# Kernel optimization log

Hardware: AMD Instinct MI355X
Metric: run time of the kernel (lower is better)

## Reference

```python
import jax, jax.numpy as jnp
import numpy as np

R = 16  # hypernetwork low rank


def _gru(x, W_ih, W_hh, b_ih, b_hh):
    # torch-style GRU (gate order: reset, update, new), batch_first. x: (B,N,D) -> (B,N,H)
    H = W_hh.shape[1]
    xp = jnp.einsum('bnd,gd->bng', x, W_ih) + b_ih            # (B,N,3H), hoisted out of scan
    xp = jnp.moveaxis(xp, 1, 0)                               # (N,B,3H)

    def step(h, xpt):
        gh = h @ W_hh.T + b_hh
        ir, iz, inn = jnp.split(xpt, 3, axis=-1)
        hr, hz, hn = jnp.split(gh, 3, axis=-1)
        r = jax.nn.sigmoid(ir + hr)
        z = jax.nn.sigmoid(iz + hz)
        n = jnp.tanh(inn + r * hn)
        h = (1.0 - z) * n + z * h
        return h, h

    h0 = jnp.zeros((x.shape[0], H), x.dtype)
    _, hs = jax.lax.scan(step, h0, xp)
    return jnp.moveaxis(hs, 0, 1)


def _assoc_scan(inputs, gates):
    # h_t = gates_t * h_{t-1} + inputs_t along the last axis (parallel associative scan)
    def combine(left, right):
        a1, b1 = left
        a2, b2 = right
        return a1 * a2, b1 * a2 + b2
    _, h = jax.lax.associative_scan(combine, (gates, inputs), axis=-1)
    return h


def setup_inputs() -> dict:
    key = jax.random.key(0)
    ks = jax.random.split(key, 18)
    B, N, D = 4, 2048, 512
    H3, Dh, Do = 3 * D, 1024, 2 * R * D
    s = 0.05
    inp = {
        'residual_stream': jax.random.normal(ks[0], (B, N, D), jnp.float32),
        'eps': jax.random.normal(ks[1], (B, N, D), jnp.float32),
        'ap_W_ih': jax.random.normal(ks[2], (H3, D)) * s,
        'ap_W_hh': jax.random.normal(ks[3], (H3, D)) * s,
        'ap_b_ih': jax.random.normal(ks[4], (H3,)) * s,
        'ap_b_hh': jax.random.normal(ks[5], (H3,)) * s,
        'su_W_ih': jax.random.normal(ks[6], (H3, D)) * s,
        'su_W_hh': jax.random.normal(ks[7], (H3, D)) * s,
        'su_b_ih': jax.random.normal(ks[8], (H3,)) * s,
        'su_b_hh': jax.random.normal(ks[9], (H3,)) * s,
        'readout_W': jax.random.normal(ks[10], (2 * D, D)) * s,
        'readout_b': jax.random.normal(ks[11], (2 * D,)) * s,
        'beta_W': jax.random.normal(ks[12], (D, D)) * s,
        'dec_W1': jax.random.normal(ks[13], (Dh, D)) * s,
        'dec_b1': jax.random.normal(ks[14], (Dh,)) * s,
        'dec_W2': jax.random.normal(ks[15], (Do, Dh)) * s,
        'dec_b2': jax.random.normal(ks[16], (Do,)) * s,
    }
    return inp


def reference(residual_stream, eps, ap_W_ih, ap_W_hh, ap_b_ih, ap_b_hh,
              su_W_ih, su_W_hh, su_b_ih, su_b_hh, readout_W, readout_b,
              beta_W, dec_W1, dec_b1, dec_W2, dec_b2):
    # non-discovery path: discovery_phase=False, hard_switch=False
    B, N, D = residual_stream.shape

    # action proposer GRU + Readout (mean / log_var, reparameterized sample)
    h = _gru(residual_stream, ap_W_ih, ap_W_hh, ap_b_ih, ap_b_hh)
    action_dist = (h @ readout_W.T + readout_b).reshape(B, N, D, 2)
    mean, log_var = action_dist[..., 0], action_dist[..., 1]
    sampled_action = mean + jnp.exp(0.5 * log_var) * eps      # (B,N,D)

    # switching unit -> per-latent-dim switch gate beta in (0,1)
    su = _gru(residual_stream, su_W_ih, su_W_hh, su_b_ih, su_b_hh)
    switch_beta = jax.nn.sigmoid(su @ beta_W.T)               # (B,N,D)

    # rearrange 'b n d -> (b d) n'
    intent = jnp.moveaxis(sampled_action, 1, 2).reshape(B * D, N)
    beta = jnp.moveaxis(switch_beta, 1, 2).reshape(B * D, N)
    forget = 1.0 - beta
    gated = _assoc_scan(intent * forget, beta)                # h_t = beta_t*h_{t-1} + (intent*forget)_t
    gated = jnp.moveaxis(gated.reshape(B, D, N), 1, 2)        # (B,N,D)

    # decoder MLP (depth=1): Linear -> SiLU -> Linear
    hdec = jax.nn.silu(gated @ dec_W1.T + dec_b1)             # (B,N,1024)
    dout = hdec @ dec_W2.T + dec_b2                           # (B,N,2*R*D)

    # '... (two d r) -> two ... d r'
    w = dout.reshape(B, N, 2, D, R)
    w1, w2 = w[..., 0, :, :], w[..., 1, :, :]                 # (B,N,D,R) each

    # control_i = g_i * sum_j sum_r w1_{i r} w2_{j r}  (fused; avoids (B,N,D,D) materialization)
    s = w2.sum(axis=-2)                                       # (B,N,R)
    t = jnp.einsum('bndr,bnr->bnd', w1, s)                    # (B,N,D)
    control_signal = gated * t

    modified = residual_stream + control_signal
    vae_kl_loss = jnp.zeros((), residual_stream.dtype)
    return modified, action_dist, sampled_action, vae_kl_loss
```

## Files before the change

### kernel.cpp

```cpp
#include <hip/hip_runtime.h>
#include <hip/hip_bf16.h>

typedef unsigned short ushort_t;
typedef unsigned long long u64_t;
typedef __attribute__((ext_vector_type(4))) float f32x4;
typedef __attribute__((ext_vector_type(8))) short short8;
typedef __attribute__((ext_vector_type(4))) unsigned int u32x4;
typedef __attribute__((ext_vector_type(4))) ushort_t u16x4;

#define BB 4
#define NN 2048
#define DD 512
#define H3 1536
#define SENT 0x7FC0ull

__device__ __forceinline__ ushort_t f2bf(float f) {
    union { float f; unsigned u; } v; v.f = f;
    unsigned r = v.u + 0x7FFFu + ((v.u >> 16) & 1u);
    return (ushort_t)(r >> 16);
}
__device__ __forceinline__ float sigm(float x) { return 1.f / (1.f + __expf(-x)); }
__device__ __forceinline__ float tanhx(float x) { return 1.f - 2.f / (__expf(2.f * x) + 1.f); }
__device__ __forceinline__ f32x4 bf4_to_f32(u64_t v) {
    f32x4 r;
#pragma unroll
    for (int i = 0; i < 4; ++i) {
        union { unsigned u; float f; } c;
        c.u = (unsigned)((v >> (16 * i)) & 0xFFFFull) << 16;
        r[i] = c.f;
    }
    return r;
}

__global__ __launch_bounds__(256) void k_cvt(const float* __restrict__ src, ushort_t* __restrict__ dst, int n4) {
    int i = blockIdx.x * 256 + threadIdx.x;
    if (i < n4) {
        f32x4 f = *(const f32x4*)(src + 4 * (size_t)i);
        u16x4 u;
#pragma unroll
        for (int r = 0; r < 4; ++r) u[r] = f2bf(f[r]);
        *(u16x4*)(dst + 4 * (size_t)i) = u;
    }
}

__global__ __launch_bounds__(256) void k_fill(u32x4* __restrict__ dst, int n16) {
    int i = blockIdx.x * 256 + threadIdx.x;
    if (i < n16) dst[i] = (u32x4){0x7FC07FC0u, 0x7FC07FC0u, 0x7FC07FC0u, 0x7FC07FC0u};
}

__global__ __launch_bounds__(256) void k_w2s(const float* __restrict__ W2, const float* __restrict__ b2,
                                             ushort_t* __restrict__ W2s, float* __restrict__ b2s) {
    int gid = blockIdx.x * 256 + threadIdx.x;
    int r = gid >> 10, k = gid & 1023;
    float s = 0.f;
    for (int d = 0; d < 512; ++d) s += W2[(size_t)(8192 + d * 16 + r) * 1024 + k];
    W2s[r * 1024 + k] = f2bf(s);
    if (gid < 16) {
        float sb = 0.f;
        for (int d = 0; d < 512; ++d) sb += b2[8192 + d * 16 + gid];
        b2s[gid] = sb;
    }
}

template <int BIAS, int ACT, int OUTBF, int REMAP>
__global__ __launch_bounds__(256) void k_gemm(const ushort_t* __restrict__ A, const ushort_t* __restrict__ W,
                                              const float* __restrict__ bias, float* __restrict__ Cf,
                                              ushort_t* __restrict__ Cbf, int M, int N, int K) {
    __shared__ __align__(16) ushort_t As[128 * 72];
    __shared__ __align__(16) ushort_t Bs[128 * 72];
    const int tid = threadIdx.x;
    const int lane = tid & 63, wave = tid >> 6;
    const int col = lane & 15, g4 = lane >> 4;
    const int wm = wave >> 1, wn = wave & 1;
    const int m0 = blockIdx.y * 128, n0 = blockIdx.x * 128;

    f32x4 acc[4][4];
#pragma unroll
    for (int i = 0; i < 4; ++i)
#pragma unroll
        for (int j = 0; j < 4; ++j) acc[i][j] = (f32x4){0.f, 0.f, 0.f, 0.f};

    for (int k0 = 0; k0 < K; k0 += 64) {
#pragma unroll
        for (int c = 0; c < 4; ++c) {
            int cid = tid + 256 * c;
            int row = cid >> 3, c8 = cid & 7;
            u32x4 va = *(const u32x4*)(A + (size_t)(m0 + row) * K + k0 + c8 * 8);
            *(u32x4*)(&As[row * 72 + c8 * 8]) = va;
            u32x4 vb = (u32x4){0u, 0u, 0u, 0u};
            if (n0 + row < N) vb = *(const u32x4*)(W + (size_t)(n0 + row) * K + k0 + c8 * 8);
            *(u32x4*)(&Bs[row * 72 + c8 * 8]) = vb;
        }
        __syncthreads();
#pragma unroll
        for (int ks = 0; ks < 2; ++ks) {
            short8 af[4], bf_[4];
#pragma unroll
            for (int i = 0; i < 4; ++i)
                af[i] = *(const short8*)(&As[(wm * 64 + i * 16 + col) * 72 + ks * 32 + g4 * 8]);
#pragma unroll
            for (int j = 0; j < 4; ++j)
                bf_[j] = *(const short8*)(&Bs[(wn * 64 + j * 16 + col) * 72 + ks * 32 + g4 * 8]);
#pragma unroll
            for (int i = 0; i < 4; ++i)
#pragma unroll
                for (int j = 0; j < 4; ++j)
                    acc[i][j] = __builtin_amdgcn_mfma_f32_16x16x32_bf16(af[i], bf_[j], acc[i][j], 0, 0, 0);
        }
        __syncthreads();
    }
#pragma unroll
    for (int j = 0; j < 4; ++j) {
        int n = n0 + wn * 64 + j * 16 + col;
        if (n >= N) continue;
        float bv = 0.f;
        if (BIAS) bv = bias[n];
#pragma unroll
        for (int i = 0; i < 4; ++i) {
#pragma unroll
            for (int r = 0; r < 4; ++r) {
                int m = m0 + wm * 64 + i * 16 + g4 * 4 + r;
                size_t mr = REMAP ? ((size_t)(m & 3) * 2048 + (m >> 2)) : (size_t)m;
                float v = acc[i][j][r] + bv;
                if (ACT == 1) v = sigm(v);
                else if (ACT == 2) v = v * sigm(v);
                if (OUTBF) Cbf[mr * N + n] = f2bf(v);
                else Cf[mr * N + n] = v;
            }
        }
    }
}

__global__ __launch_bounds__(512, 1) void k_gru(const float* __restrict__ Whh0, const float* __restrict__ Whh1,
                                                const float* __restrict__ bhh0, const float* __restrict__ bhh1,
                                                const ushort_t* __restrict__ xpb0, const ushort_t* __restrict__ xpb1,
                                                ushort_t* __restrict__ hseq0, ushort_t* __restrict__ hseq1) {
    __shared__ __align__(16) ushort_t HB[2][4 * 520];
    const int gru = blockIdx.x >> 2;
    const int wg = blockIdx.x & 3;
    const float* Whh = gru ? Whh1 : Whh0;
    const float* bhh = gru ? bhh1 : bhh0;
    const ushort_t* xpb = gru ? xpb1 : xpb0;
    ushort_t* hseq = gru ? hseq1 : hseq0;

    const int tid = threadIdx.x;
    const int wave = tid >> 6, lane = tid & 63;
    const int col = lane & 15, g4 = lane >> 4;
    const int u = wg * 8 + wave;
    const int c0 = u * 16;

    const bool gvalid = (tid < 384);
    const int uo = tid >> 4;
    const int gu = (uo < wg * 8) ? uo : uo + 8;
    const int gb = (tid >> 2) & 3, gq = tid & 3;
    const int g_u64 = gu * 4 + gq;
    const int g_lds = gb * 520 + gu * 16 + gq * 4;

    short8 af[3][16];
#pragma unroll
    for (int m = 0; m < 3; ++m) {
        int grow = m * 512 + c0 + col;
        const float* wr = Whh + (size_t)grow * 512;
#pragma unroll
        for (int q = 0; q < 16; ++q) {
            int k = q * 32 + g4 * 8;
            f32x4 f0 = *(const f32x4*)(wr + k);
            f32x4 f1 = *(const f32x4*)(wr + k + 4);
            short8 v;
#pragma unroll
            for (int i = 0; i < 4; ++i) v[i] = (short)f2bf(f0[i]);
#pragma unroll
            for (int i = 0; i < 4; ++i) v[4 + i] = (short)f2bf(f1[i]);
            af[m][q] = v;
        }
    }

    const bool active = (col < 4);
    const int b = active ? col : 0;
    const int j0 = c0 + g4 * 4;
    f32x4 bhr = {0.f, 0.f, 0.f, 0.f}, bhz = bhr, bhn = bhr;
    if (active) {
        bhr = *(const f32x4*)(bhh + j0);
        bhz = *(const f32x4*)(bhh + 512 + j0);
        bhn = *(const f32x4*)(bhh + 1024 + j0);
    }
    float hold[4] = {0.f, 0.f, 0.f, 0.f};
    long long budget = 1LL << 21;

    u64_t xr8 = 0, xz8 = 0, xn8 = 0;
    if (active) {
        const ushort_t* xpt = xpb + ((size_t)b * NN) * 1536;
        xr8 = *(const u64_t*)(xpt + j0);
        xz8 = *(const u64_t*)(xpt + 512 + j0);
        xn8 = *(const u64_t*)(xpt + 1024 + j0);
    }

    for (int t = 0; t < NN; ++t) {
        u64_t xrn = 0, xzn = 0, xnn = 0;
        if (active && t + 1 < NN) {
            const ushort_t* xpt = xpb + ((size_t)b * NN + t + 1) * 1536;
            xrn = *(const u64_t*)(xpt + j0);
            xzn = *(const u64_t*)(xpt + 512 + j0);
            xnn = *(const u64_t*)(xpt + 1024 + j0);
        }
        if (t > 0) {
            if (gvalid) {
                const u64_t* gp = (const u64_t*)hseq + ((size_t)(t - 1) * 4 + gb) * 128 + g_u64;
                u64_t v = __hip_atomic_load(gp, __ATOMIC_RELAXED, __HIP_MEMORY_SCOPE_AGENT);
                while ((v & 0xFFFFull) == SENT && --budget >= 0)
                    v = __hip_atomic_load(gp, __ATOMIC_RELAXED, __HIP_MEMORY_SCOPE_AGENT);
                *(u64_t*)(&HB[(t - 1) & 1][g_lds]) = v;
            }
        }
        __syncthreads();
        f32x4 a0 = {0.f, 0.f, 0.f, 0.f}, a1 = a0, a2 = a0;
        if (t > 0) {
            const ushort_t* hb = &HB[(t - 1) & 1][(col & 3) * 520];
            short8 bf_[16];
#pragma unroll
            for (int q = 0; q < 16; ++q) bf_[q] = *(const short8*)(hb + q * 32 + g4 * 8);
#pragma unroll
            for (int q = 0; q < 16; ++q) {
                a0 = __builtin_amdgcn_mfma_f32_16x16x32_bf16(af[0][q], bf_[q], a0, 0, 0, 0);
                a1 = __builtin_amdgcn_mfma_f32_16x16x32_bf16(af[1][q], bf_[q], a1, 0, 0, 0);
                a2 = __builtin_amdgcn_mfma_f32_16x16x32_bf16(af[2][q], bf_[q], a2, 0, 0, 0);
            }
        }
        if (active) {
            f32x4 xr = bf4_to_f32(xr8), xz = bf4_to_f32(xz8), xn = bf4_to_f32(xn8);
            u16x4 pk;
#pragma unroll
            for (int r = 0; r < 4; ++r) {
                float rr = sigm(xr[r] + bhr[r] + a0[r]);
                float zz = sigm(xz[r] + bhz[r] + a1[r]);
                float nnv = tanhx(xn[r] + rr * (a2[r] + bhn[r]));
                float hv = (1.f - zz) * nnv + zz * hold[r];
                hold[r] = hv;
                pk[r] = f2bf(hv);
            }
            union { u16x4 p; u64_t u; } pc;
            pc.p = pk;
            __hip_atomic_store((u64_t*)(hseq + ((size_t)t * 4 + b) * 512 + j0), pc.u, __ATOMIC_RELAXED,
                               __HIP_MEMORY_SCOPE_AGENT);
            *(u64_t*)(&HB[t & 1][b * 520 + j0]) = pc.u;
        }
        xr8 = xrn; xz8 = xzn; xn8 = xnn;
    }
}

__global__ __launch_bounds__(256) void k_sample(const float* __restrict__ ad, const float* __restrict__ eps,
                                                float* __restrict__ out2, int n) {
    int i = blockIdx.x * 256 + threadIdx.x;
    if (i < n) {
        float mean = ad[2 * (size_t)i];
        float lv = ad[2 * (size_t)i + 1];
        out2[i] = mean + __expf(0.5f * lv) * eps[i];
    }
}

#define NC 32
#define LCH 64
__global__ __launch_bounds__(512) void k_scan1(const float* __restrict__ beta_tm, const float* __restrict__ intent,
                                               float* __restrict__ Asum, float* __restrict__ Bsum) {
    int d = threadIdx.x;
    int b = blockIdx.x / NC, c = blockIdx.x % NC;
    float A = 1.f, Bc = 0.f;
    for (int i = 0; i < LCH; ++i) {
        size_t t = (size_t)c * LCH + i;
        float a = beta_tm[(t * 4 + b) * 512 + d];
        float x = intent[((size_t)b * NN + t) * 512 + d] * (1.f - a);
        A *= a;
        Bc = a * Bc + x;
    }
    Asum[(b * NC + c) * 512 + d] = A;
    Bsum[(b * NC + c) * 512 + d] = Bc;
}
__global__ __launch_bounds__(512) void k_scan2(const float* __restrict__ Asum, const float* __restrict__ Bsum,
                                               float* __restrict__ P) {
    int d = threadIdx.x;
    int b = blockIdx.x;
    float carry = 0.f;
    for (int c = 0; c < NC; ++c) {
        int o = (b * NC + c) * 512 + d;
        P[o] = carry;
        carry = Asum[o] * carry + Bsum[o];
    }
}
__global__ __launch_bounds__(512) void k_scan3(const float* __restrict__ beta_tm, const float* __restrict__ intent,
                                               const float* __restrict__ P, float* __restrict__ gated,
                                               ushort_t* __restrict__ gated_bf) {
    int d = threadIdx.x;
    int b = blockIdx.x / NC, c = blockIdx.x % NC;
    float h = P[(b * NC + c) * 512 + d];
    for (int i = 0; i < LCH; ++i) {
        size_t t = (size_t)c * LCH + i;
        size_t idx = ((size_t)b * NN + t) * 512 + d;
        float a = beta_tm[(t * 4 + b) * 512 + d];
        float x = intent[idx] * (1.f - a);
        h = a * h + x;
        gated[idx] = h;
        gated_bf[idx] = f2bf(h);
    }
}

__global__ __launch_bounds__(256) void k_contract(const float* __restrict__ w1s, const float* __restrict__ s,
                                                  const float* __restrict__ gated, const float* __restrict__ resid,
                                                  float* __restrict__ out0, int blk) {
    int gid = blockIdx.x * 256 + threadIdx.x;
    int ml = gid >> 9, d = gid & 511;
    size_t m = (size_t)blk * 1024 + ml;
    const f32x4* wp = (const f32x4*)(w1s + ((size_t)ml * 8192 + d * 16));
    const f32x4* sp = (const f32x4*)(s + m * 16);
    float t = 0.f;
#pragma unroll
    for (int q = 0; q < 4; ++q) {
        f32x4 w = wp[q], sv = sp[q];
        t += w[0] * sv[0] + w[1] * sv[1] + w[2] * sv[2] + w[3] * sv[3];
    }
    size_t o = m * 512 + d;
    out0[o] = resid[o] + gated[o] * t;
}

extern "C" void kernel_launch(void* const* d_in, const int* in_sizes, int n_in, void* d_out, int out_size, void* d_ws,
                              size_t ws_size, hipStream_t stream) {
    const float* x = (const float*)d_in[0];
    const float* eps = (const float*)d_in[1];
    const float* ap_W_ih = (const float*)d_in[2];
    const float* ap_W_hh = (const float*)d_in[3];
    const float* ap_b_ih = (const float*)d_in[4];
    const float* ap_b_hh = (const float*)d_in[5];
    const float* su_W_ih = (const float*)d_in[6];
    const float* su_W_hh = (const float*)d_in[7];
    const float* su_b_ih = (const float*)d_in[8];
    const float* su_b_hh = (const float*)d_in[9];
    const float* readout_W = (const float*)d_in[10];
    const float* readout_b = (const float*)d_in[11];
    const float* beta_W = (const float*)d_in[12];
    const float* dec_W1 = (const float*)d_in[13];
    const float* dec_b1 = (const float*)d_in[14];
    const float* dec_W2 = (const float*)d_in[15];
    const float* dec_b2 = (const float*)d_in[16];

    float* out = (float*)d_out;
    float* out_ad = out + (size_t)4194304;
    float* out_sa = out + (size_t)12582912;

    char* ws = (char*)d_ws;
    size_t off = 0;
    auto alloc = [&](size_t bytes) -> void* {
        off = (off + 255) & ~(size_t)255;
        void* p = ws + off;
        off += bytes;
        return p;
    };
    ushort_t* x_bf = (ushort_t*)alloc((size_t)8192 * 512 * 2);
    ushort_t* wih_ap = (ushort_t*)alloc((size_t)1536 * 512 * 2);
    ushort_t* wih_su = (ushort_t*)alloc((size_t)1536 * 512 * 2);
    ushort_t* wro = (ushort_t*)alloc((size_t)1024 * 512 * 2);
    ushort_t* wbeta = (ushort_t*)alloc((size_t)512 * 512 * 2);
    ushort_t* wd1 = (ushort_t*)alloc((size_t)1024 * 512 * 2);
    ushort_t* wd2 = (ushort_t*)alloc((size_t)8192 * 1024 * 2);
    ushort_t* w2s = (ushort_t*)alloc((size_t)16 * 1024 * 2);
    float* b2s = (float*)alloc(64);
    ushort_t* hseq_ap = (ushort_t*)alloc((size_t)8192 * 512 * 2);
    ushort_t* hseq_su = (ushort_t*)alloc((size_t)8192 * 512 * 2);
    float* s_buf = (float*)alloc((size_t)8192 * 16 * 4);
    char* regionA = (char*)alloc(50331648);
    char* regionB = (char*)alloc(50331648);

    ushort_t* xpb_ap = (ushort_t*)regionA;
    ushort_t* xpb_su = (ushort_t*)regionB;
    float* beta_tm = (float*)regionA;
    float* gated = (float*)(regionA + 16777216);
    ushort_t* gated_bf = (ushort_t*)(regionA + 2 * 16777216);
    float* Asum = (float*)(regionA + 41943040);
    float* Bsum = (float*)(regionA + 41943040 + 262144);
    float* Pbuf = (float*)(regionA + 41943040 + 524288);
    ushort_t* hdec_bf = (ushort_t*)regionB;
    float* w1s = (float*)(regionB + 16777216);

    hipMemsetAsync(out + (size_t)(out_size - 1), 0, 4, stream);

    k_fill<<<2048, 256, 0, stream>>>((u32x4*)hseq_ap, 524288);
    k_fill<<<2048, 256, 0, stream>>>((u32x4*)hseq_su, 524288);

    k_cvt<<<768, 256, 0, stream>>>(ap_W_ih, wih_ap, 196608);
    k_cvt<<<768, 256, 0, stream>>>(su_W_ih, wih_su, 196608);
    k_cvt<<<512, 256, 0, stream>>>(readout_W, wro, 131072);
    k_cvt<<<256, 256, 0, stream>>>(beta_W, wbeta, 65536);
    k_cvt<<<512, 256, 0, stream>>>(dec_W1, wd1, 131072);
    k_cvt<<<8192, 256, 0, stream>>>(dec_W2, wd2, 2097152);
    k_cvt<<<4096, 256, 0, stream>>>(x, x_bf, 1048576);
    k_w2s<<<64, 256, 0, stream>>>(dec_W2, dec_b2, w2s, b2s);

    k_gemm<1, 0, 1, 0><<<dim3(12, 64), 256, 0, stream>>>(x_bf, wih_ap, ap_b_ih, nullptr, xpb_ap, 8192, 1536, 512);
    k_gemm<1, 0, 1, 0><<<dim3(12, 64), 256, 0, stream>>>(x_bf, wih_su, su_b_ih, nullptr, xpb_su, 8192, 1536, 512);

    k_gru<<<8, 512, 0, stream>>>(ap_W_hh, su_W_hh, ap_b_hh, su_b_hh, xpb_ap, xpb_su, hseq_ap, hseq_su);

    k_gemm<1, 0, 0, 1><<<dim3(8, 64), 256, 0, stream>>>(hseq_ap, wro, readout_b, out_ad, nullptr, 8192, 1024, 512);
    k_sample<<<16384, 256, 0, stream>>>(out_ad, eps, out_sa, 4194304);

    k_gemm<0, 1, 0, 0><<<dim3(4, 64), 256, 0, stream>>>(hseq_su, wbeta, nullptr, beta_tm, nullptr, 8192, 512, 512);

    k_scan1<<<4 * NC, 512, 0, stream>>>(beta_tm, out_sa, Asum, Bsum);
    k_scan2<<<4, 512, 0, stream>>>(Asum, Bsum, Pbuf);
    k_scan3<<<4 * NC, 512, 0, stream>>>(beta_tm, out_sa, Pbuf, gated, gated_bf);

    k_gemm<1, 2, 1, 0><<<dim3(8, 64), 256, 0, stream>>>(gated_bf, wd1, dec_b1, nullptr, hdec_bf, 8192, 1024, 512);

    k_gemm<1, 0, 0, 0><<<dim3(1, 64), 256, 0, stream>>>(hdec_bf, w2s, b2s, s_buf, nullptr, 8192, 16, 1024);

    for (int blk = 0; blk < 8; ++blk) {
        k_gemm<1, 0, 0, 0><<<dim3(64, 8), 256, 0, stream>>>(hdec_bf + (size_t)blk * 1024 * 1024, wd2, dec_b2, w1s,
                                                            nullptr, 1024, 8192, 1024);
        k_contract<<<2048, 256, 0, stream>>>(w1s, s_buf, gated, x, out, blk);
    }
}
```

Measured before the change: 6.376 ms.

## Fuse w1 rank contraction into decoder GEMM epilogue, drop w1s buffer

The large decoder GEMM (8192x8192x1024) now applies bias, multiplies by the per-row s vector, reduces over the rank-16 group with cross-lane shuffles, and writes the final residual+gated*t output directly. This removes the fp32 w1s intermediate (32 MB per block written then reread) and the eight-chunk loop of separate GEMM and contract launches, replacing them with one full-size launch. The cost is a heavier epilogue with shuffles and scattered single-lane stores of s, gated, resid, and out, and only col==0 lanes doing the writes.

```diff
diff --git a/kernel.cpp b/kernel.cpp
--- a/kernel.cpp
+++ b/kernel.cpp
@@ -62,10 +62,12 @@
     }
 }
 
-template <int BIAS, int ACT, int OUTBF, int REMAP>
+template <int BIAS, int ACT, int OUTBF, int REMAP, int CONTRACT>
 __global__ __launch_bounds__(256) void k_gemm(const ushort_t* __restrict__ A, const ushort_t* __restrict__ W,
                                               const float* __restrict__ bias, float* __restrict__ Cf,
-                                              ushort_t* __restrict__ Cbf, int M, int N, int K) {
+                                              ushort_t* __restrict__ Cbf, int M, int N, int K,
+                                              const float* __restrict__ s, const float* __restrict__ gated,
+                                              const float* __restrict__ resid, float* __restrict__ out0) {
     __shared__ __align__(16) ushort_t As[128 * 72];
     __shared__ __align__(16) ushort_t Bs[128 * 72];
     const int tid = threadIdx.x;
@@ -108,6 +110,31 @@
                     acc[i][j] = __builtin_amdgcn_mfma_f32_16x16x32_bf16(af[i], bf_[j], acc[i][j], 0, 0, 0);
         }
         __syncthreads();
+    }
+    if (CONTRACT) {
+#pragma unroll
+        for (int j = 0; j < 4; ++j) {
+            int nb = n0 + wn * 64 + j * 16;
+            int d = nb >> 4;
+            float bv = bias[nb + col];
+#pragma unroll
+            for (int i = 0; i < 4; ++i) {
+#pragma unroll
+                for (int r = 0; r < 4; ++r) {
+                    int m = m0 + wm * 64 + i * 16 + g4 * 4 + r;
+                    float v = (acc[i][j][r] + bv) * s[(size_t)m * 16 + col];
+                    v += __shfl_xor(v, 1, 16);
+                    v += __shfl_xor(v, 2, 16);
+                    v += __shfl_xor(v, 4, 16);
+                    v += __shfl_xor(v, 8, 16);
+                    if (col == 0) {
+                        size_t o = (size_t)m * 512 + d;
+                        out0[o] = resid[o] + gated[o] * v;
+                    }
+                }
+            }
+        }
+        return;
     }
 #pragma unroll
     for (int j = 0; j < 4; ++j) {
@@ -301,24 +328,6 @@
         gated[idx] = h;
         gated_bf[idx] = f2bf(h);
     }
-}
-
-__global__ __launch_bounds__(256) void k_contract(const float* __restrict__ w1s, const float* __restrict__ s,
-                                                  const float* __restrict__ gated, const float* __restrict__ resid,
-                                                  float* __restrict__ out0, int blk) {
-    int gid = blockIdx.x * 256 + threadIdx.x;
-    int ml = gid >> 9, d = gid & 511;
-    size_t m = (size_t)blk * 1024 + ml;
-    const f32x4* wp = (const f32x4*)(w1s + ((size_t)ml * 8192 + d * 16));
-    const f32x4* sp = (const f32x4*)(s + m * 16);
-    float t = 0.f;
-#pragma unroll
-    for (int q = 0; q < 4; ++q) {
-        f32x4 w = wp[q], sv = sp[q];
-        t += w[0] * sv[0] + w[1] * sv[1] + w[2] * sv[2] + w[3] * sv[3];
-    }
-    size_t o = m * 512 + d;
-    out0[o] = resid[o] + gated[o] * t;
 }
 
 extern "C" void kernel_launch(void* const* d_in, const int* in_sizes, int n_in, void* d_out, int out_size, void* d_ws,
@@ -377,7 +386,6 @@
     float* Bsum = (float*)(regionA + 41943040 + 262144);
     float* Pbuf = (float*)(regionA + 41943040 + 524288);
     ushort_t* hdec_bf = (ushort_t*)regionB;
-    float* w1s = (float*)(regionB + 16777216);
 
     hipMemsetAsync(out + (size_t)(out_size - 1), 0, 4, stream);
 
@@ -393,27 +401,30 @@
     k_cvt<<<4096, 256, 0, stream>>>(x, x_bf, 1048576);
     k_w2s<<<64, 256, 0, stream>>>(dec_W2, dec_b2, w2s, b2s);
 
-    k_gemm<1, 0, 1, 0><<<dim3(12, 64), 256, 0, stream>>>(x_bf, wih_ap, ap_b_ih, nullptr, xpb_ap, 8192, 1536, 512);
-    k_gemm<1, 0, 1, 0><<<dim3(12, 64), 256, 0, stream>>>(x_bf, wih_su, su_b_ih, nullptr, xpb_su, 8192, 1536, 512);
+    k_gemm<1, 0, 1, 0, 0><<<dim3(12, 64), 256, 0, stream>>>(x_bf, wih_ap, ap_b_ih, nullptr, xpb_ap, 8192, 1536, 512,
+                                                            nullptr, nullptr, nullptr, nullptr);
+    k_gemm<1, 0, 1, 0, 0><<<dim3(12, 64), 256, 0, stream>>>(x_bf, wih_su, su_b_ih, nullptr, xpb_su, 8192, 1536, 512,
+                                                            nullptr, nullptr, nullptr, nullptr);
 
     k_gru<<<8, 512, 0, stream>>>(ap_W_hh, su_W_hh, ap_b_hh, su_b_hh, xpb_ap, xpb_su, hseq_ap, hseq_su);
 
-    k_gemm<1, 0, 0, 1><<<dim3(8, 64), 256, 0, stream>>>(hseq_ap, wro, readout_b, out_ad, nullptr, 8192, 1024, 512);
+    k_gemm<1, 0, 0, 1, 0><<<dim3(8, 64), 256, 0, stream>>>(hseq_ap, wro, readout_b, out_ad, nullptr, 8192, 1024, 512,
+                                                           nullptr, nullptr, nullptr, nullptr);
     k_sample<<<16384, 256, 0, stream>>>(out_ad, eps, out_sa, 4194304);
 
-    k_gemm<0, 1, 0, 0><<<dim3(4, 64), 256, 0, stream>>>(hseq_su, wbeta, nullptr, beta_tm, nullptr, 8192, 512, 512);
+    k_gemm<0, 1, 0, 0, 0><<<dim3(4, 64), 256, 0, stream>>>(hseq_su, wbeta, nullptr, beta_tm, nullptr, 8192, 512, 512,
+                                                           nullptr, nullptr, nullptr, nullptr);
 
     k_scan1<<<4 * NC, 512, 0, stream>>>(beta_tm, out_sa, Asum, Bsum);
     k_scan2<<<4, 512, 0, stream>>>(Asum, Bsum, Pbuf);
     k_scan3<<<4 * NC, 512, 0, stream>>>(beta_tm, out_sa, Pbuf, gated, gated_bf);
 
-    k_gemm<1, 2, 1, 0><<<dim3(8, 64), 256, 0, stream>>>(gated_bf, wd1, dec_b1, nullptr, hdec_bf, 8192, 1024, 512);
-
-    k_gemm<1, 0, 0, 0><<<dim3(1, 64), 256, 0, stream>>>(hdec_bf, w2s, b2s, s_buf, nullptr, 8192, 16, 1024);
-
-    for (int blk = 0; blk < 8; ++blk) {
-        k_gemm<1, 0, 0, 0><<<dim3(64, 8), 256, 0, stream>>>(hdec_bf + (size_t)blk * 1024 * 1024, wd2, dec_b2, w1s,
-                                                            nullptr, 1024, 8192, 1024);
-        k_contract<<<2048, 256, 0, stream>>>(w1s, s_buf, gated, x, out, blk);
-    }
-}
+    k_gemm<1, 2, 1, 0, 0><<<dim3(8, 64), 256, 0, stream>>>(gated_bf, wd1, dec_b1, nullptr, hdec_bf, 8192, 1024, 512,
+                                                           nullptr, nullptr, nullptr, nullptr);
+
+    k_gemm<1, 0, 0, 0, 0><<<dim3(1, 64), 256, 0, stream>>>(hdec_bf, w2s, b2s, s_buf, nullptr, 8192, 16, 1024,
+                                                           nullptr, nullptr, nullptr, nullptr);
+
+    k_gemm<1, 0, 0, 0, 1><<<dim3(64, 64), 256, 0, stream>>>(hdec_bf, wd2, dec_b2, nullptr, nullptr, 8192, 8192, 1024,
+                                                            s_buf, gated, x, out);
+}
```

New measurement: 6.415 ms. Within noise of the previous version (+0.6%).
